# Kernel tuning notes

Measured on AMD Instinct MI355X. Metric: run time of the kernel, lower is better.

Reference implementation:

```python
import jax, jax.numpy as jnp
import numpy as np

D_MODEL = 1024
NUM_HEADS = 16
D_HEAD = D_MODEL // NUM_HEADS


def setup_inputs() -> dict:
    key = jax.random.key(0)
    ks = jax.random.split(key, 9)
    s = 1.0 / np.sqrt(D_MODEL)
    return {
        "x": jax.random.normal(ks[0], (2, 2048, D_MODEL), dtype=jnp.float32),
        "Wq": jax.random.normal(ks[1], (D_MODEL, D_MODEL), dtype=jnp.float32) * s,
        "bq": jnp.zeros((D_MODEL,), dtype=jnp.float32),
        "Wk": jax.random.normal(ks[2], (D_MODEL, D_MODEL), dtype=jnp.float32) * s,
        "bk": jnp.zeros((D_MODEL,), dtype=jnp.float32),
        "Wv": jax.random.normal(ks[3], (D_MODEL, D_MODEL), dtype=jnp.float32) * s,
        "bv": jnp.zeros((D_MODEL,), dtype=jnp.float32),
        "Wo": jax.random.normal(ks[4], (D_MODEL, D_MODEL), dtype=jnp.float32) * s,
        "bo": jnp.zeros((D_MODEL,), dtype=jnp.float32),
    }


def reference(x, Wq, bq, Wk, bk, Wv, bv, Wo, bo):
    B, S, D = x.shape
    H, Dh = NUM_HEADS, D_HEAD

    def split_heads(t):  # [B,S,D] -> [B,H,S,Dh]
        return t.reshape(B, S, H, Dh).transpose(0, 2, 1, 3)

    # Linear layers: y = x @ W^T + b (torch nn.Linear convention)
    Q = split_heads(x @ Wq.T + bq)
    K = split_heads(x @ Wk.T + bk)
    V = split_heads(x @ Wv.T + bv)

    scale = 1.0 / jnp.sqrt(jnp.asarray(Dh, dtype=x.dtype))
    scores = jnp.einsum("bhqd,bhkd->bhqk", Q, K) * scale  # [B,H,S,S]
    attn = jax.nn.softmax(scores, axis=-1)
    context = jnp.einsum("bhqk,bhkd->bhqd", attn, V)  # [B,H,S,Dh]
    context = context.transpose(0, 2, 1, 3).reshape(B, S, D)
    return context @ Wo.T + bo
```

## Files before the change

### kernel.cpp

```cpp
#include <hip/hip_runtime.h>


#define T_TOK 4096
#define DM    1024
#define SQ    2048
#define NH    16
#define DH    64

typedef unsigned short u16;
typedef unsigned int   u32;
typedef __bf16 bf16x8 __attribute__((ext_vector_type(8)));
typedef float  f32x4  __attribute__((ext_vector_type(4)));

__device__ __forceinline__ u16 f2bf(float f) {
  u32 u = __builtin_bit_cast(u32, f);
  u32 r = (u + 0x7FFFu + ((u >> 16) & 1u)) >> 16;
  return (u16)r;
}

#if __has_builtin(__builtin_amdgcn_cvt_pk_bf16_f32)
typedef __bf16 bf16x2 __attribute__((ext_vector_type(2)));
__device__ __forceinline__ u32 pk2bf(float a, float b) {
  bf16x2 h = __builtin_amdgcn_cvt_pk_bf16_f32(a, b);
  return __builtin_bit_cast(u32, h);
}
#else
__device__ __forceinline__ u32 pk2bf(float a, float b) {
  return (u32)f2bf(a) | ((u32)f2bf(b) << 16);
}
#endif

__device__ __forceinline__ void gld16(const void* g, void* l) {
  __builtin_amdgcn_global_load_lds(
      (const __attribute__((address_space(1))) u32*)g,
      (__attribute__((address_space(3))) u32*)l, 16, 0, 0);
}

__global__ void cast_bf16_kernel(const float* __restrict__ x,
    const float* __restrict__ w0, const float* __restrict__ w1,
    const float* __restrict__ w2, const float* __restrict__ w3,
    u16* __restrict__ xb, u16* __restrict__ o0, u16* __restrict__ o1,
    u16* __restrict__ o2, u16* __restrict__ o3)
{
  const float* src; u16* dst; int n;
  switch (blockIdx.y) {
    case 0:  src = x;  dst = xb; n = T_TOK * DM; break;
    case 1:  src = w0; dst = o0; n = DM * DM; break;
    case 2:  src = w1; dst = o1; n = DM * DM; break;
    case 3:  src = w2; dst = o2; n = DM * DM; break;
    default: src = w3; dst = o3; n = DM * DM; break;
  }
  const int stride = gridDim.x * blockDim.x;
  for (int i = blockIdx.x * blockDim.x + threadIdx.x; i * 4 < n; i += stride) {
    float4 v = ((const float4*)src)[i];
    ushort4 o;
    o.x = f2bf(v.x); o.y = f2bf(v.y); o.z = f2bf(v.z); o.w = f2bf(v.w);
    ((ushort4*)dst)[i] = o;
  }
}

__device__ __forceinline__ void gemm_core_128x128(
    const u16* __restrict__ Ab, const u16* __restrict__ Bb, f32x4 acc[4][4])
{
  __shared__ __align__(16) u16 As[128 * 32];
  __shared__ __align__(16) u16 Bs[128 * 32];
  const int tid = threadIdx.x, lane = tid & 63, w = tid >> 6;
  const int waveM = w >> 1, waveN = w & 1;
  const int srow = lane >> 2, sch = lane & 3;
  const int col = lane & 15, quad = lane >> 4;

  for (int k0 = 0; k0 < DM; k0 += 32) {
    #pragma unroll
    for (int i = 0; i < 2; ++i) {
      const int rb = w * 32 + i * 16;
      gld16(Ab + (size_t)(rb + srow) * DM + k0 + sch * 8, &As[rb * 32]);
      gld16(Bb + (size_t)(rb + srow) * DM + k0 + sch * 8, &Bs[rb * 32]);
    }
    __syncthreads();
    bf16x8 af[4], bg[4];
    #pragma unroll
    for (int i = 0; i < 4; ++i)
      af[i] = *(const bf16x8*)&As[(waveM * 64 + i * 16 + col) * 32 + quad * 8];
    #pragma unroll
    for (int j = 0; j < 4; ++j)
      bg[j] = *(const bf16x8*)&Bs[(waveN * 64 + j * 16 + col) * 32 + quad * 8];
    #pragma unroll
    for (int i = 0; i < 4; ++i) {
      #pragma unroll
      for (int j = 0; j < 4; ++j)
        acc[i][j] = __builtin_amdgcn_mfma_f32_16x16x32_bf16(af[i], bg[j], acc[i][j], 0, 0, 0);
    }
    __syncthreads();
  }
}

__global__ __launch_bounds__(256) void gemm_qkv_kernel(
    const u16* __restrict__ xb,
    const u16* __restrict__ Wqb, const u16* __restrict__ Wkb, const u16* __restrict__ Wvb,
    const float* __restrict__ bq, const float* __restrict__ bk, const float* __restrict__ bv,
    u16* __restrict__ Qs, u16* __restrict__ Kh, u16* __restrict__ Vt)
{
  __shared__ __align__(16) u16 tr[128 * 136];
  const int z = blockIdx.z;
  const u16*   Wb   = (z == 0) ? Wqb : (z == 1) ? Wkb : Wvb;
  const float* bias = (z == 0) ? bq  : (z == 1) ? bk  : bv;
  const float scale = (z == 0) ? 0.18033688011112042f : 1.0f;

  f32x4 acc[4][4];
  const f32x4 zf = {0.f, 0.f, 0.f, 0.f};
  #pragma unroll
  for (int i = 0; i < 4; ++i) {
    #pragma unroll
    for (int j = 0; j < 4; ++j) acc[i][j] = zf;
  }
  gemm_core_128x128(xb + (size_t)(blockIdx.y * 128) * DM,
                    Wb + (size_t)(blockIdx.x * 128) * DM, acc);

  const int tid = threadIdx.x;
  const int lane = tid & 63, w = tid >> 6;
  const int waveM = w >> 1, waveN = w & 1;
  const int col = lane & 15, quad = lane >> 4;
  const int rowBase = blockIdx.y * 128 + waveM * 64;
  const int colBase = blockIdx.x * 128 + waveN * 64;
  if (z == 2) {
    #pragma unroll
    for (int j = 0; j < 4; ++j) {
      const int cl = waveN * 64 + j * 16 + col;
      const float bb = bias[blockIdx.x * 128 + cl];
      #pragma unroll
      for (int i = 0; i < 4; ++i) {
        const int tl = waveM * 64 + i * 16 + quad * 4;
        ushort4 pk;
        pk.x = f2bf(acc[i][j][0] + bb); pk.y = f2bf(acc[i][j][1] + bb);
        pk.z = f2bf(acc[i][j][2] + bb); pk.w = f2bf(acc[i][j][3] + bb);
        *(ushort4*)&tr[cl * 136 + tl] = pk;
      }
    }
    __syncthreads();
    const int t0 = blockIdx.y * 128;
    const int b = t0 >> 11, sBase = t0 & 2047;
    #pragma unroll
    for (int rep = 0; rep < 8; ++rep) {
      const int chunk = rep * 256 + tid;
      const int row = chunk >> 4, off = (chunk & 15) * 8;
      const int c = blockIdx.x * 128 + row;
      const int h = c >> 6, d = c & 63;
      uint4 v = *(const uint4*)&tr[row * 136 + off];
      *(uint4*)&Vt[((size_t)(b * NH + h) * DH + d) * SQ + sBase + off] = v;
    }
  } else {
    u16* out = (z == 0) ? Qs : Kh;
    #pragma unroll
    for (int j = 0; j < 4; ++j) {
      const int c = colBase + j * 16 + col;
      const float bb = bias[c];
      const int h = c >> 6, d = c & 63;
      #pragma unroll
      for (int i = 0; i < 4; ++i) {
        #pragma unroll
        for (int r = 0; r < 4; ++r) {
          const int t = rowBase + i * 16 + quad * 4 + r;
          const int b = t >> 11, s = t & 2047;
          out[((size_t)(b * NH + h) * SQ + s) * DH + d] = f2bf((acc[i][j][r] + bb) * scale);
        }
      }
    }
  }
}

__global__ __launch_bounds__(256, 4) void attn_kernel(
    const u16* __restrict__ Qs, const u16* __restrict__ Kh,
    const u16* __restrict__ Vt, u16* __restrict__ ctx)
{
  __shared__ __align__(16) u16 Kt[2][64 * 64];
  __shared__ __align__(16) u16 Vl[2][64 * 64];
  __shared__ __align__(16) u16 Pt[64 * 64];
  const int tid = threadIdx.x, lane = tid & 63, w = tid >> 6;
  const int col = lane & 15, quad = lane >> 4;
  const int srow = lane >> 3;
  const int sgrn = (lane & 7) ^ srow;
  const int bh = blockIdx.y, q0 = blockIdx.x * 64;
  const u16* Qb = Qs + ((size_t)bh * SQ + q0) * DH;
  const u16* Kb = Kh + (size_t)bh * SQ * DH;
  const u16* Vb = Vt + (size_t)bh * DH * SQ;
  const int sw = col & 7;

  bf16x8 qreg[2];
  #pragma unroll
  for (int c = 0; c < 2; ++c)
    qreg[c] = *(const bf16x8*)(Qb + (size_t)(w * 16 + col) * DH + c * 32 + quad * 8);

  #pragma unroll
  for (int i = 0; i < 2; ++i) {
    const int rb = w * 16 + i * 8;
    gld16(Kb + (size_t)(rb + srow) * DH + sgrn * 8, &Kt[0][rb * 64]);
    gld16(Vb + (size_t)(rb + srow) * SQ + sgrn * 8, &Vl[0][rb * 64]);
  }

  const f32x4 zf = {0.f, 0.f, 0.f, 0.f};
  f32x4 cacc[4];
  float l_s = 0.f;
  #pragma unroll
  for (int mt = 0; mt < 4; ++mt) cacc[mt] = zf;
  __syncthreads();

  for (int kt = 0; kt < SQ / 64; ++kt) {
    const int cur = kt & 1;
    if (kt + 1 < SQ / 64) {
      const int nxt = cur ^ 1, s1 = (kt + 1) * 64;
      #pragma unroll
      for (int i = 0; i < 2; ++i) {
        const int rb = w * 16 + i * 8;
        gld16(Kb + (size_t)(s1 + rb + srow) * DH + sgrn * 8, &Kt[nxt][rb * 64]);
        gld16(Vb + (size_t)(rb + srow) * SQ + s1 + sgrn * 8, &Vl[nxt][rb * 64]);
      }
    }

    f32x4 sacc[4];
    #pragma unroll
    for (int mt = 0; mt < 4; ++mt) sacc[mt] = zf;
    #pragma unroll
    for (int c = 0; c < 2; ++c) {
      bf16x8 ak[4];
      #pragma unroll
      for (int mt = 0; mt < 4; ++mt)
        ak[mt] = *(const bf16x8*)&Kt[cur][(mt * 16 + col) * 64
                                          + (((c * 4 + quad) ^ sw) * 8)];
      #pragma unroll
      for (int mt = 0; mt < 4; ++mt)
        sacc[mt] = __builtin_amdgcn_mfma_f32_16x16x32_bf16(
            ak[mt], qreg[c], sacc[mt], 0, 0, 0);
    }

    const int qloc = w * 16 + col;
    #pragma unroll
    for (int mt = 0; mt < 4; ++mt) {
      float p0 = __builtin_amdgcn_exp2f(sacc[mt][0] - 24.0f);
      float p1 = __builtin_amdgcn_exp2f(sacc[mt][1] - 24.0f);
      float p2 = __builtin_amdgcn_exp2f(sacc[mt][2] - 24.0f);
      float p3 = __builtin_amdgcn_exp2f(sacc[mt][3] - 24.0f);
      l_s += (p0 + p1) + (p2 + p3);
      uint2 pk;
      pk.x = pk2bf(p0, p1);
      pk.y = pk2bf(p2, p3);
      *(uint2*)&Pt[qloc * 64 + (((mt * 2 + (quad >> 1)) ^ sw) * 8)
                   + (quad & 1) * 4] = pk;
    }

    #pragma unroll
    for (int c = 0; c < 2; ++c) {
      bf16x8 av[4];
      bf16x8 bp = *(const bf16x8*)&Pt[(w * 16 + col) * 64
                                      + (((c * 4 + quad) ^ sw) * 8)];
      #pragma unroll
      for (int mt = 0; mt < 4; ++mt)
        av[mt] = *(const bf16x8*)&Vl[cur][(mt * 16 + col) * 64
                                          + (((c * 4 + quad) ^ sw) * 8)];
      #pragma unroll
      for (int mt = 0; mt < 4; ++mt)
        cacc[mt] = __builtin_amdgcn_mfma_f32_16x16x32_bf16(
            av[mt], bp, cacc[mt], 0, 0, 0);
    }
    __syncthreads();
  }

  const int b = bh >> 4, h = bh & 15;
  float l = l_s;
  l += __shfl_xor(l, 16, 64);
  l += __shfl_xor(l, 32, 64);
  const float inv = 1.0f / l;
  const int s = q0 + w * 16 + col;
  #pragma unroll
  for (int mt = 0; mt < 4; ++mt) {
    uint2 pk;
    pk.x = pk2bf(cacc[mt][0] * inv, cacc[mt][1] * inv);
    pk.y = pk2bf(cacc[mt][2] * inv, cacc[mt][3] * inv);
    *(uint2*)&ctx[(size_t)(b * SQ + s) * DM + h * DH + mt * 16 + quad * 4] = pk;
  }
}

__global__ __launch_bounds__(256) void gemm_out_kernel(
    const u16* __restrict__ ctx, const u16* __restrict__ Wob,
    const float* __restrict__ bo, float* __restrict__ out)
{
  __shared__ __align__(16) u16 As[128 * 32];
  __shared__ __align__(16) u16 Bs[64 * 32];
  const u16* Ab = ctx + (size_t)(blockIdx.y * 128) * DM;
  const u16* Bb = Wob + (size_t)(blockIdx.x * 64) * DM;
  const int tid = threadIdx.x, lane = tid & 63, w = tid >> 6;
  const int waveM = w >> 1, waveN = w & 1;
  const int srow = lane >> 2, sch = lane & 3;
  const int col = lane & 15, quad = lane >> 4;

  f32x4 acc[4][2];
  const f32x4 zf = {0.f, 0.f, 0.f, 0.f};
  #pragma unroll
  for (int i = 0; i < 4; ++i) {
    #pragma unroll
    for (int j = 0; j < 2; ++j) acc[i][j] = zf;
  }

  for (int k0 = 0; k0 < DM; k0 += 32) {
    #pragma unroll
    for (int i = 0; i < 2; ++i) {
      const int rb = w * 32 + i * 16;
      gld16(Ab + (size_t)(rb + srow) * DM + k0 + sch * 8, &As[rb * 32]);
    }
    {
      const int rb = w * 16;
      gld16(Bb + (size_t)(rb + srow) * DM + k0 + sch * 8, &Bs[rb * 32]);
    }
    __syncthreads();
    bf16x8 af[4], bg[2];
    #pragma unroll
    for (int i = 0; i < 4; ++i)
      af[i] = *(const bf16x8*)&As[(waveM * 64 + i * 16 + col) * 32 + quad * 8];
    #pragma unroll
    for (int j = 0; j < 2; ++j)
      bg[j] = *(const bf16x8*)&Bs[(waveN * 32 + j * 16 + col) * 32 + quad * 8];
    #pragma unroll
    for (int i = 0; i < 4; ++i) {
      #pragma unroll
      for (int j = 0; j < 2; ++j)
        acc[i][j] = __builtin_amdgcn_mfma_f32_16x16x32_bf16(af[i], bg[j], acc[i][j], 0, 0, 0);
    }
    __syncthreads();
  }

  const int rowBase = blockIdx.y * 128 + waveM * 64;
  const int colBase = blockIdx.x * 64 + waveN * 32;
  #pragma unroll
  for (int j = 0; j < 2; ++j) {
    const int c = colBase + j * 16 + col;
    const float bb = bo[c];
    #pragma unroll
    for (int i = 0; i < 4; ++i) {
      #pragma unroll
      for (int r = 0; r < 4; ++r) {
        const int t = rowBase + i * 16 + quad * 4 + r;
        out[(size_t)t * DM + c] = acc[i][j][r] + bb;
      }
    }
  }
}

extern "C" void kernel_launch(void* const* d_in, const int* in_sizes, int n_in,
                              void* d_out, int out_size, void* d_ws, size_t ws_size,
                              hipStream_t stream) {
  const float* x  = (const float*)d_in[0];
  const float* Wq = (const float*)d_in[1];
  const float* bq = (const float*)d_in[2];
  const float* Wk = (const float*)d_in[3];
  const float* bk = (const float*)d_in[4];
  const float* Wv = (const float*)d_in[5];
  const float* bv = (const float*)d_in[6];
  const float* Wo = (const float*)d_in[7];
  const float* bo = (const float*)d_in[8];

  char* ws = (char*)d_ws;
  u16* xb  = (u16*)(ws);
  u16* Wqb = (u16*)(ws + (8ull  << 20));
  u16* Wkb = (u16*)(ws + (10ull << 20));
  u16* Wvb = (u16*)(ws + (12ull << 20));
  u16* Wob = (u16*)(ws + (14ull << 20));
  u16* Qs  = (u16*)(ws + (16ull << 20));
  u16* Kh  = (u16*)(ws + (24ull << 20));
  u16* Vt  = (u16*)(ws + (32ull << 20));
  u16* ctx = xb;

  cast_bf16_kernel<<<dim3(256, 5), 256, 0, stream>>>(x, Wq, Wk, Wv, Wo,
                                                     xb, Wqb, Wkb, Wvb, Wob);
  gemm_qkv_kernel<<<dim3(8, 32, 3), 256, 0, stream>>>(xb, Wqb, Wkb, Wvb,
                                                      bq, bk, bv, Qs, Kh, Vt);
  attn_kernel<<<dim3(32, 32), 256, 0, stream>>>(Qs, Kh, Vt, ctx);
  gemm_out_kernel<<<dim3(16, 32), 256, 0, stream>>>(ctx, Wob, bo, (float*)d_out);
  (void)in_sizes; (void)n_in; (void)out_size; (void)ws_size;
}
```

Before: 219.2 us.

## Rework attention kernel to 32x32 MFMA with key-split waves and register P

The attention kernel now uses 32x32x16 MFMA tiles and processes 128 keys per iteration. Each wave takes a 32-key slice for all 64 queries instead of owning 16 query rows. The P matrix is passed between the two lane halves with shuffles instead of an LDS round trip. Partial context sums and row sums are then reduced across waves through shared memory at the end. The LDS double buffering is dropped for a single buffer with a sync per tile, and occupancy is lowered to 3 blocks, which may expose load latency.

```diff
diff --git a/kernel.cpp b/kernel.cpp
--- a/kernel.cpp
+++ b/kernel.cpp
@@ -11,6 +11,8 @@
 typedef unsigned int   u32;
 typedef __bf16 bf16x8 __attribute__((ext_vector_type(8)));
 typedef float  f32x4  __attribute__((ext_vector_type(4)));
+typedef float  f32x16 __attribute__((ext_vector_type(16)));
+typedef u32    u32x4  __attribute__((ext_vector_type(4)));
 
 __device__ __forceinline__ u16 f2bf(float f) {
   u32 u = __builtin_bit_cast(u32, f);
@@ -168,114 +170,162 @@
   }
 }
 
-__global__ __launch_bounds__(256, 4) void attn_kernel(
+__global__ __launch_bounds__(256, 3) void attn_kernel(
     const u16* __restrict__ Qs, const u16* __restrict__ Kh,
     const u16* __restrict__ Vt, u16* __restrict__ ctx)
 {
-  __shared__ __align__(16) u16 Kt[2][64 * 64];
-  __shared__ __align__(16) u16 Vl[2][64 * 64];
-  __shared__ __align__(16) u16 Pt[64 * 64];
+  __shared__ __align__(16) char smem[33 * 1024];
+  u16*   Kt   = (u16*)smem;
+  u16*   Vl   = (u16*)(smem + 16384);
+  f32x4* red  = (f32x4*)smem;
+  float* lred = (float*)(smem + 32768);
+
   const int tid = threadIdx.x, lane = tid & 63, w = tid >> 6;
-  const int col = lane & 15, quad = lane >> 4;
-  const int srow = lane >> 3;
-  const int sgrn = (lane & 7) ^ srow;
+  const int l31 = lane & 31, h = lane >> 5;
   const int bh = blockIdx.y, q0 = blockIdx.x * 64;
   const u16* Qb = Qs + ((size_t)bh * SQ + q0) * DH;
   const u16* Kb = Kh + (size_t)bh * SQ * DH;
   const u16* Vb = Vt + (size_t)bh * DH * SQ;
-  const int sw = col & 7;
-
-  bf16x8 qreg[2];
-  #pragma unroll
-  for (int c = 0; c < 2; ++c)
-    qreg[c] = *(const bf16x8*)(Qb + (size_t)(w * 16 + col) * DH + c * 32 + quad * 8);
-
-  #pragma unroll
-  for (int i = 0; i < 2; ++i) {
-    const int rb = w * 16 + i * 8;
-    gld16(Kb + (size_t)(rb + srow) * DH + sgrn * 8, &Kt[0][rb * 64]);
-    gld16(Vb + (size_t)(rb + srow) * SQ + sgrn * 8, &Vl[0][rb * 64]);
-  }
-
-  const f32x4 zf = {0.f, 0.f, 0.f, 0.f};
-  f32x4 cacc[4];
-  float l_s = 0.f;
-  #pragma unroll
-  for (int mt = 0; mt < 4; ++mt) cacc[mt] = zf;
-  __syncthreads();
-
-  for (int kt = 0; kt < SQ / 64; ++kt) {
-    const int cur = kt & 1;
-    if (kt + 1 < SQ / 64) {
-      const int nxt = cur ^ 1, s1 = (kt + 1) * 64;
-      #pragma unroll
-      for (int i = 0; i < 2; ++i) {
-        const int rb = w * 16 + i * 8;
-        gld16(Kb + (size_t)(s1 + rb + srow) * DH + sgrn * 8, &Kt[nxt][rb * 64]);
-        gld16(Vb + (size_t)(rb + srow) * SQ + s1 + sgrn * 8, &Vl[nxt][rb * 64]);
-      }
-    }
-
-    f32x4 sacc[4];
-    #pragma unroll
-    for (int mt = 0; mt < 4; ++mt) sacc[mt] = zf;
-    #pragma unroll
-    for (int c = 0; c < 2; ++c) {
-      bf16x8 ak[4];
-      #pragma unroll
-      for (int mt = 0; mt < 4; ++mt)
-        ak[mt] = *(const bf16x8*)&Kt[cur][(mt * 16 + col) * 64
-                                          + (((c * 4 + quad) ^ sw) * 8)];
-      #pragma unroll
-      for (int mt = 0; mt < 4; ++mt)
-        sacc[mt] = __builtin_amdgcn_mfma_f32_16x16x32_bf16(
-            ak[mt], qreg[c], sacc[mt], 0, 0, 0);
-    }
-
-    const int qloc = w * 16 + col;
-    #pragma unroll
-    for (int mt = 0; mt < 4; ++mt) {
-      float p0 = __builtin_amdgcn_exp2f(sacc[mt][0] - 24.0f);
-      float p1 = __builtin_amdgcn_exp2f(sacc[mt][1] - 24.0f);
-      float p2 = __builtin_amdgcn_exp2f(sacc[mt][2] - 24.0f);
-      float p3 = __builtin_amdgcn_exp2f(sacc[mt][3] - 24.0f);
-      l_s += (p0 + p1) + (p2 + p3);
-      uint2 pk;
-      pk.x = pk2bf(p0, p1);
-      pk.y = pk2bf(p2, p3);
-      *(uint2*)&Pt[qloc * 64 + (((mt * 2 + (quad >> 1)) ^ sw) * 8)
-                   + (quad & 1) * 4] = pk;
-    }
-
-    #pragma unroll
-    for (int c = 0; c < 2; ++c) {
-      bf16x8 av[4];
-      bf16x8 bp = *(const bf16x8*)&Pt[(w * 16 + col) * 64
-                                      + (((c * 4 + quad) ^ sw) * 8)];
-      #pragma unroll
-      for (int mt = 0; mt < 4; ++mt)
-        av[mt] = *(const bf16x8*)&Vl[cur][(mt * 16 + col) * 64
-                                          + (((c * 4 + quad) ^ sw) * 8)];
-      #pragma unroll
-      for (int mt = 0; mt < 4; ++mt)
-        cacc[mt] = __builtin_amdgcn_mfma_f32_16x16x32_bf16(
-            av[mt], bp, cacc[mt], 0, 0, 0);
-    }
-    __syncthreads();
-  }
-
-  const int b = bh >> 4, h = bh & 15;
-  float l = l_s;
-  l += __shfl_xor(l, 16, 64);
-  l += __shfl_xor(l, 32, 64);
-  const float inv = 1.0f / l;
-  const int s = q0 + w * 16 + col;
-  #pragma unroll
-  for (int mt = 0; mt < 4; ++mt) {
-    uint2 pk;
-    pk.x = pk2bf(cacc[mt][0] * inv, cacc[mt][1] * inv);
-    pk.y = pk2bf(cacc[mt][2] * inv, cacc[mt][3] * inv);
-    *(uint2*)&ctx[(size_t)(b * SQ + s) * DM + h * DH + mt * 16 + quad * 4] = pk;
+
+  bf16x8 qreg[2][4];
+  #pragma unroll
+  for (int qt = 0; qt < 2; ++qt) {
+    #pragma unroll
+    for (int ks = 0; ks < 4; ++ks)
+      qreg[qt][ks] = *(const bf16x8*)(Qb + (size_t)(qt * 32 + l31) * DH
+                                         + ks * 16 + h * 8);
+  }
+
+  f32x16 cacc[2][2];
+  #pragma unroll
+  for (int dt = 0; dt < 2; ++dt)
+    #pragma unroll
+    for (int qt = 0; qt < 2; ++qt)
+      #pragma unroll
+      for (int e = 0; e < 16; ++e) cacc[dt][qt][e] = 0.f;
+  float l_s[2] = {0.f, 0.f};
+
+  for (int kt = 0; kt < SQ / 128; ++kt) {
+    const int s0 = kt * 128;
+    #pragma unroll
+    for (int i = 0; i < 4; ++i) {
+      const int rb = w * 32 + i * 8;
+      const int rowloc = rb + (lane >> 3);
+      const int sg = (lane & 7) ^ (lane >> 3) ^ ((rb >> 3) & 3);
+      gld16(Kb + (size_t)(s0 + rowloc) * DH + sg * 8, &Kt[rb * 64]);
+    }
+    #pragma unroll
+    for (int i = 0; i < 4; ++i) {
+      const int rb = w * 16 + i * 4;
+      const int rowloc = rb + (lane >> 4);
+      const int sg = (lane & 15) ^ (rowloc & 15);
+      gld16(Vb + (size_t)rowloc * SQ + s0 + sg * 8, &Vl[rb * 128]);
+    }
+    __syncthreads();
+
+    f32x16 sacc[2];
+    #pragma unroll
+    for (int qt = 0; qt < 2; ++qt)
+      #pragma unroll
+      for (int e = 0; e < 16; ++e) sacc[qt][e] = 0.f;
+    #pragma unroll
+    for (int ks = 0; ks < 4; ++ks) {
+      const int row = w * 32 + l31;
+      const int gp = (2 * ks + h) ^ (l31 & 7) ^ ((l31 >> 3) & 3);
+      bf16x8 kf = *(const bf16x8*)&Kt[row * 64 + gp * 8];
+      sacc[0] = __builtin_amdgcn_mfma_f32_32x32x16_bf16(kf, qreg[0][ks], sacc[0], 0, 0, 0);
+      sacc[1] = __builtin_amdgcn_mfma_f32_32x32x16_bf16(kf, qreg[1][ks], sacc[1], 0, 0, 0);
+    }
+
+    u32 Pp[2][4][2];
+    #pragma unroll
+    for (int qt = 0; qt < 2; ++qt) {
+      float p[16];
+      #pragma unroll
+      for (int e = 0; e < 16; ++e) {
+        p[e] = __builtin_amdgcn_exp2f(sacc[qt][e] - 24.0f);
+        l_s[qt] += p[e];
+      }
+      #pragma unroll
+      for (int rg = 0; rg < 4; ++rg) {
+        Pp[qt][rg][0] = pk2bf(p[4 * rg + 0], p[4 * rg + 1]);
+        Pp[qt][rg][1] = pk2bf(p[4 * rg + 2], p[4 * rg + 3]);
+      }
+    }
+
+    #pragma unroll
+    for (int ks = 0; ks < 2; ++ks) {
+      bf16x8 pf[2];
+      #pragma unroll
+      for (int qt = 0; qt < 2; ++qt) {
+        u32 own0 = h ? Pp[qt][2 * ks + 1][0] : Pp[qt][2 * ks][0];
+        u32 own1 = h ? Pp[qt][2 * ks + 1][1] : Pp[qt][2 * ks][1];
+        u32 snd0 = h ? Pp[qt][2 * ks][0] : Pp[qt][2 * ks + 1][0];
+        u32 snd1 = h ? Pp[qt][2 * ks][1] : Pp[qt][2 * ks + 1][1];
+        u32 rcv0 = (u32)__shfl_xor((int)snd0, 32, 64);
+        u32 rcv1 = (u32)__shfl_xor((int)snd1, 32, 64);
+        u32x4 fw;
+        fw.x = h ? rcv0 : own0;
+        fw.y = h ? rcv1 : own1;
+        fw.z = h ? own0 : rcv0;
+        fw.w = h ? own1 : rcv1;
+        pf[qt] = __builtin_bit_cast(bf16x8, fw);
+      }
+      #pragma unroll
+      for (int dt = 0; dt < 2; ++dt) {
+        const int row = dt * 32 + l31;
+        const int gp = (4 * w + 2 * ks + h) ^ (row & 15);
+        bf16x8 vf = *(const bf16x8*)&Vl[row * 128 + gp * 8];
+        cacc[dt][0] = __builtin_amdgcn_mfma_f32_32x32x16_bf16(vf, pf[0], cacc[dt][0], 0, 0, 0);
+        cacc[dt][1] = __builtin_amdgcn_mfma_f32_32x32x16_bf16(vf, pf[1], cacc[dt][1], 0, 0, 0);
+      }
+    }
+    __syncthreads();
+  }
+
+  float lq[2];
+  #pragma unroll
+  for (int qt = 0; qt < 2; ++qt) {
+    lq[qt] = l_s[qt] + __shfl_xor(l_s[qt], 32, 64);
+    if (h == 0) lred[(w * 2 + qt) * 32 + l31] = lq[qt];
+  }
+  const int b = bh >> 4, hd = bh & 15;
+  #pragma unroll
+  for (int qt = 0; qt < 2; ++qt) {
+    __syncthreads();
+    #pragma unroll
+    for (int dt = 0; dt < 2; ++dt) {
+      #pragma unroll
+      for (int c = 0; c < 4; ++c) {
+        f32x4 ch;
+        ch[0] = cacc[dt][qt][4 * c + 0]; ch[1] = cacc[dt][qt][4 * c + 1];
+        ch[2] = cacc[dt][qt][4 * c + 2]; ch[3] = cacc[dt][qt][4 * c + 3];
+        red[((w * 2 + dt) * 4 + c) * 64 + lane] = ch;
+      }
+    }
+    __syncthreads();
+    const int dt = w >> 1, c0 = (w & 1) * 2;
+    f32x4 sum[2];
+    #pragma unroll
+    for (int j = 0; j < 2; ++j) { sum[j][0]=0; sum[j][1]=0; sum[j][2]=0; sum[j][3]=0; }
+    #pragma unroll
+    for (int sw = 0; sw < 4; ++sw) {
+      #pragma unroll
+      for (int j = 0; j < 2; ++j)
+        sum[j] += red[((sw * 2 + dt) * 4 + c0 + j) * 64 + lane];
+    }
+    float lsum = lred[(0 * 2 + qt) * 32 + l31] + lred[(1 * 2 + qt) * 32 + l31]
+               + lred[(2 * 2 + qt) * 32 + l31] + lred[(3 * 2 + qt) * 32 + l31];
+    const float inv = 1.0f / lsum;
+    const int s = q0 + qt * 32 + l31;
+    #pragma unroll
+    for (int j = 0; j < 2; ++j) {
+      const int d0 = dt * 32 + (c0 + j) * 8 + 4 * h;
+      ushort4 pk;
+      pk.x = f2bf(sum[j][0] * inv); pk.y = f2bf(sum[j][1] * inv);
+      pk.z = f2bf(sum[j][2] * inv); pk.w = f2bf(sum[j][3] * inv);
+      *(ushort4*)&ctx[(size_t)(b * SQ + s) * DM + hd * DH + d0] = pk;
+    }
   }
 }
 
```

Result: slower. 242.7 us (+10.7%).
